# Performance work log

Measured on AMD Instinct MI355X. Metric: run time of the kernel, lower is better.

The kernel has to match this reference:

```python
import jax, jax.numpy as jnp
from jax import lax
import numpy as np

SOFT_LOCAL_MAX_SIZE = 3
PAD = SOFT_LOCAL_MAX_SIZE // 2


def setup_inputs() -> dict:
    key = jax.random.key(0)
    k1, k2 = jax.random.split(key)
    x = jax.random.normal(k1, (16, 64, 256, 256), dtype=jnp.float32)
    W = jax.random.normal(k2, (2, 64), dtype=jnp.float32) * 0.1  # 1x1 conv weight [out_c, in_c]
    b = jnp.zeros((2,), dtype=jnp.float32)
    return {"x": x, "W": W, "b": b}


def reference(x, W, b):
    # 1x1 conv == channel contraction
    y = jnp.einsum('bchw,oc->bohw', x, W) + b[None, :, None, None]
    e = jnp.exp(y)  # [B, 2, H, W]
    # replicate pad + 3x3 box SUM (avg_pool * k^2 == sum over window)
    p = jnp.pad(e, ((0, 0), (0, 0), (PAD, PAD), (PAD, PAD)), mode='edge')
    sum_exp = lax.reduce_window(
        p, jnp.float32(0.0), lax.add,
        window_dimensions=(1, 1, SOFT_LOCAL_MAX_SIZE, SOFT_LOCAL_MAX_SIZE),
        window_strides=(1, 1, 1, 1), padding='VALID')
    sum_exp = jnp.sum(sum_exp, axis=1, keepdims=True)  # channel sum -> [B,1,H,W]
    local_max_score = e / sum_exp
    return local_max_score[:, 0, :, :]  # [B, H, W]
```

## Files before the change

kernel.cpp:

```cpp
#include <hip/hip_runtime.h>
#include <math.h>

#define BB 16
#define CC 64
#define HH 256
#define WW 256
#define HWX (HH * WW)
#define NPIX (BB * HWX)

__global__ __launch_bounds__(256) void conv_exp_kernel(
    const float* __restrict__ x,
    const float* __restrict__ Wt,
    const float* __restrict__ bias,
    float* __restrict__ e0,
    float* __restrict__ s)
{
    __shared__ float w0[CC];
    __shared__ float w1[CC];
    const int tid = threadIdx.x;
    if (tid < CC) {
        w0[tid] = Wt[tid];
        w1[tid] = Wt[CC + tid];
    }
    __syncthreads();

    const float b0 = bias[0];
    const float b1 = bias[1];

    const long long p4 = (long long)blockIdx.x * blockDim.x + tid;
    const long long base = p4 * 4;
    if (base >= NPIX) return;
    const int bimg = (int)(base >> 16);
    const int q    = (int)(base & 65535);
    const float* xp = x + (long long)bimg * CC * HWX + q;

    float4 a0 = make_float4(b0, b0, b0, b0);
    float4 a1 = make_float4(b1, b1, b1, b1);

    #pragma unroll 8
    for (int c = 0; c < CC; ++c) {
        const float4 v = *(const float4*)(xp + (long long)c * HWX);
        const float wc0 = w0[c];
        const float wc1 = w1[c];
        a0.x = fmaf(v.x, wc0, a0.x);
        a0.y = fmaf(v.y, wc0, a0.y);
        a0.z = fmaf(v.z, wc0, a0.z);
        a0.w = fmaf(v.w, wc0, a0.w);
        a1.x = fmaf(v.x, wc1, a1.x);
        a1.y = fmaf(v.y, wc1, a1.y);
        a1.z = fmaf(v.z, wc1, a1.z);
        a1.w = fmaf(v.w, wc1, a1.w);
    }

    float4 E0, E1, S;
    E0.x = __expf(a0.x); E0.y = __expf(a0.y); E0.z = __expf(a0.z); E0.w = __expf(a0.w);
    E1.x = __expf(a1.x); E1.y = __expf(a1.y); E1.z = __expf(a1.z); E1.w = __expf(a1.w);
    S.x = E0.x + E1.x; S.y = E0.y + E1.y; S.z = E0.z + E1.z; S.w = E0.w + E1.w;

    *(float4*)(e0 + base) = E0;
    *(float4*)(s  + base) = S;
}

__global__ __launch_bounds__(256) void box_div_kernel(
    const float* __restrict__ e0,
    const float* __restrict__ s,
    float* __restrict__ out)
{
    const int idx = blockIdx.x * blockDim.x + threadIdx.x;
    if (idx >= NPIX) return;
    const int bimg = idx >> 16;
    const int q    = idx & 65535;
    const int h = q >> 8;
    const int w = q & 255;

    const int hm = (h > 0)      ? h - 1 : 0;
    const int hp = (h < HH - 1) ? h + 1 : HH - 1;
    const int wm = (w > 0)      ? w - 1 : 0;
    const int wp = (w < WW - 1) ? w + 1 : WW - 1;

    const float* sb = s + bimg * HWX;
    const int rm = hm * WW, r0 = h * WW, rp = hp * WW;

    const float sum =
        sb[rm + wm] + sb[rm + w] + sb[rm + wp] +
        sb[r0 + wm] + sb[r0 + w] + sb[r0 + wp] +
        sb[rp + wm] + sb[rp + w] + sb[rp + wp];

    out[idx] = e0[idx] / sum;
}

extern "C" void kernel_launch(void* const* d_in, const int* in_sizes, int n_in,
                              void* d_out, int out_size, void* d_ws, size_t ws_size,
                              hipStream_t stream) {
    const float* x    = (const float*)d_in[0];
    const float* Wt   = (const float*)d_in[1];
    const float* bias = (const float*)d_in[2];
    float* out = (float*)d_out;

    float* e0 = (float*)d_ws;
    float* s  = e0 + NPIX;

    {
        const int threads = 256;
        const int total = NPIX / 4;
        const int blocks = (total + threads - 1) / threads;
        conv_exp_kernel<<<blocks, threads, 0, stream>>>(x, Wt, bias, e0, s);
    }
    {
        const int threads = 256;
        const int blocks = (NPIX + threads - 1) / threads;
        box_div_kernel<<<blocks, threads, 0, stream>>>(e0, s, out);
    }
}
```

Measured before the change: 367.8 us.

## Fuse conv-exp and box-sum-divide into one row-tiled kernel with shared-memory halo

Replaces the two-kernel pipeline with a single kernel where each block computes a 16-row tile plus one halo row above and below. The block computes exp values into shared memory and then does the 3x3 box sum and divide locally. This removes the global write and re-read of the intermediate e0 and sum arrays and one kernel launch. In exchange it recomputes the channel contraction for halo rows (18/16 of the x reads) and launches only 256 large blocks of 576 threads, which may limit occupancy and latency hiding on the 64-channel read.

New measurement: 368.8 us. Within noise of the previous version (+0.3%).

```diff
diff --git a/kernel.cpp b/kernel.cpp
--- a/kernel.cpp
+++ b/kernel.cpp
@@ -1,92 +1,119 @@
 #include <hip/hip_runtime.h>
 #include <math.h>
 
-#define BB 16
 #define CC 64
 #define HH 256
 #define WW 256
 #define HWX (HH * WW)
-#define NPIX (BB * HWX)
+#define BB 16
+#define TH 16
+#define TROWS (TH + 2)
 
-__global__ __launch_bounds__(256) void conv_exp_kernel(
+__global__ __launch_bounds__(576) void fused_sdm_kernel(
     const float* __restrict__ x,
     const float* __restrict__ Wt,
     const float* __restrict__ bias,
-    float* __restrict__ e0,
-    float* __restrict__ s)
+    float* __restrict__ out)
 {
     __shared__ float w0[CC];
     __shared__ float w1[CC];
+    __shared__ float sS[TROWS][WW];
+    __shared__ float sE[TROWS][WW];
+
     const int tid = threadIdx.x;
-    if (tid < CC) {
-        w0[tid] = Wt[tid];
-        w1[tid] = Wt[CC + tid];
-    }
+    if (tid < CC)           w0[tid]      = Wt[tid];
+    else if (tid < 2 * CC)  w1[tid - CC] = Wt[tid];
     __syncthreads();
 
     const float b0 = bias[0];
     const float b1 = bias[1];
 
-    const long long p4 = (long long)blockIdx.x * blockDim.x + tid;
-    const long long base = p4 * 4;
-    if (base >= NPIX) return;
-    const int bimg = (int)(base >> 16);
-    const int q    = (int)(base & 65535);
-    const float* xp = x + (long long)bimg * CC * HWX + q;
+    const int bimg = blockIdx.x >> 4;
+    const int tile = blockIdx.x & 15;
+    const int h0   = tile * TH;
 
-    float4 a0 = make_float4(b0, b0, b0, b0);
-    float4 a1 = make_float4(b1, b1, b1, b1);
+    const int wg = tid & 63;
+    const int g  = tid >> 6;
+    const int w4 = wg << 2;
 
-    #pragma unroll 8
+    const int r0 = g;
+    const int r1 = g + 9;
+
+    int h_a = h0 + r0 - 1; h_a = h_a < 0 ? 0 : (h_a > HH - 1 ? HH - 1 : h_a);
+    int h_b = h0 + r1 - 1; h_b = h_b < 0 ? 0 : (h_b > HH - 1 ? HH - 1 : h_b);
+
+    const float* xb = x + (size_t)bimg * CC * HWX;
+    const int offA = h_a * WW + w4;
+    const int offB = h_b * WW + w4;
+
+    float4 A0 = make_float4(b0, b0, b0, b0);
+    float4 B0 = A0;
+    float4 A1 = make_float4(b1, b1, b1, b1);
+    float4 B1 = A1;
+
+    #pragma unroll 4
     for (int c = 0; c < CC; ++c) {
-        const float4 v = *(const float4*)(xp + (long long)c * HWX);
+        const float4 va = *(const float4*)(xb + (size_t)c * HWX + offA);
+        const float4 vb = *(const float4*)(xb + (size_t)c * HWX + offB);
         const float wc0 = w0[c];
         const float wc1 = w1[c];
-        a0.x = fmaf(v.x, wc0, a0.x);
-        a0.y = fmaf(v.y, wc0, a0.y);
-        a0.z = fmaf(v.z, wc0, a0.z);
-        a0.w = fmaf(v.w, wc0, a0.w);
-        a1.x = fmaf(v.x, wc1, a1.x);
-        a1.y = fmaf(v.y, wc1, a1.y);
-        a1.z = fmaf(v.z, wc1, a1.z);
-        a1.w = fmaf(v.w, wc1, a1.w);
+        A0.x = fmaf(va.x, wc0, A0.x);
+        A0.y = fmaf(va.y, wc0, A0.y);
+        A0.z = fmaf(va.z, wc0, A0.z);
+        A0.w = fmaf(va.w, wc0, A0.w);
+        A1.x = fmaf(va.x, wc1, A1.x);
+        A1.y = fmaf(va.y, wc1, A1.y);
+        A1.z = fmaf(va.z, wc1, A1.z);
+        A1.w = fmaf(va.w, wc1, A1.w);
+        B0.x = fmaf(vb.x, wc0, B0.x);
+        B0.y = fmaf(vb.y, wc0, B0.y);
+        B0.z = fmaf(vb.z, wc0, B0.z);
+        B0.w = fmaf(vb.w, wc0, B0.w);
+        B1.x = fmaf(vb.x, wc1, B1.x);
+        B1.y = fmaf(vb.y, wc1, B1.y);
+        B1.z = fmaf(vb.z, wc1, B1.z);
+        B1.w = fmaf(vb.w, wc1, B1.w);
     }
 
-    float4 E0, E1, S;
-    E0.x = __expf(a0.x); E0.y = __expf(a0.y); E0.z = __expf(a0.z); E0.w = __expf(a0.w);
-    E1.x = __expf(a1.x); E1.y = __expf(a1.y); E1.z = __expf(a1.z); E1.w = __expf(a1.w);
-    S.x = E0.x + E1.x; S.y = E0.y + E1.y; S.z = E0.z + E1.z; S.w = E0.w + E1.w;
+    float4 EA, EB, SA, SB;
+    EA.x = __expf(A0.x); EA.y = __expf(A0.y); EA.z = __expf(A0.z); EA.w = __expf(A0.w);
+    EB.x = __expf(B0.x); EB.y = __expf(B0.y); EB.z = __expf(B0.z); EB.w = __expf(B0.w);
+    SA.x = EA.x + __expf(A1.x); SA.y = EA.y + __expf(A1.y);
+    SA.z = EA.z + __expf(A1.z); SA.w = EA.w + __expf(A1.w);
+    SB.x = EB.x + __expf(B1.x); SB.y = EB.y + __expf(B1.y);
+    SB.z = EB.z + __expf(B1.z); SB.w = EB.w + __expf(B1.w);
 
-    *(float4*)(e0 + base) = E0;
-    *(float4*)(s  + base) = S;
-}
+    *(float4*)&sE[r0][w4] = EA;
+    *(float4*)&sS[r0][w4] = SA;
+    *(float4*)&sE[r1][w4] = EB;
+    *(float4*)&sS[r1][w4] = SB;
+    __syncthreads();
 
-__global__ __launch_bounds__(256) void box_div_kernel(
-    const float* __restrict__ e0,
-    const float* __restrict__ s,
-    float* __restrict__ out)
-{
-    const int idx = blockIdx.x * blockDim.x + threadIdx.x;
-    if (idx >= NPIX) return;
-    const int bimg = idx >> 16;
-    const int q    = idx & 65535;
-    const int h = q >> 8;
-    const int w = q & 255;
+    const int wl = (wg == 0)  ? 0      : w4 - 1;
+    const int wr = (wg == 63) ? WW - 1 : w4 + 4;
+    float* outb = out + (size_t)bimg * HWX;
 
-    const int hm = (h > 0)      ? h - 1 : 0;
-    const int hp = (h < HH - 1) ? h + 1 : HH - 1;
-    const int wm = (w > 0)      ? w - 1 : 0;
-    const int wp = (w < WW - 1) ? w + 1 : WW - 1;
+    #pragma unroll
+    for (int k = 0; k < 2; ++k) {
+        const int r = k ? r1 : r0;
+        if (r < 1 || r > TH) continue;
 
-    const float* sb = s + bimg * HWX;
-    const int rm = hm * WW, r0 = h * WW, rp = hp * WW;
-
-    const float sum =
-        sb[rm + wm] + sb[rm + w] + sb[rm + wp] +
-        sb[r0 + wm] + sb[r0 + w] + sb[r0 + wp] +
-        sb[rp + wm] + sb[rp + w] + sb[rp + wp];
-
-    out[idx] = e0[idx] / sum;
+        float cs0 = 0.f, cs1 = 0.f, cs2 = 0.f, cs3 = 0.f, cs4 = 0.f, cs5 = 0.f;
+        #pragma unroll
+        for (int dr = -1; dr <= 1; ++dr) {
+            const float4 m = *(const float4*)&sS[r + dr][w4];
+            cs0 += sS[r + dr][wl];
+            cs1 += m.x; cs2 += m.y; cs3 += m.z; cs4 += m.w;
+            cs5 += sS[r + dr][wr];
+        }
+        const float4 e = *(const float4*)&sE[r][w4];
+        float4 o;
+        o.x = e.x / (cs0 + cs1 + cs2);
+        o.y = e.y / (cs1 + cs2 + cs3);
+        o.z = e.z / (cs2 + cs3 + cs4);
+        o.w = e.w / (cs3 + cs4 + cs5);
+        *(float4*)(outb + (size_t)(h0 + r - 1) * WW + w4) = o;
+    }
 }
 
 extern "C" void kernel_launch(void* const* d_in, const int* in_sizes, int n_in,
@@ -97,18 +124,6 @@
     const float* bias = (const float*)d_in[2];
     float* out = (float*)d_out;
 
-    float* e0 = (float*)d_ws;
-    float* s  = e0 + NPIX;
-
-    {
-        const int threads = 256;
-        const int total = NPIX / 4;
-        const int blocks = (total + threads - 1) / threads;
-        conv_exp_kernel<<<blocks, threads, 0, stream>>>(x, Wt, bias, e0, s);
-    }
-    {
-        const int threads = 256;
-        const int blocks = (NPIX + threads - 1) / threads;
-        box_div_kernel<<<blocks, threads, 0, stream>>>(e0, s, out);
-    }
+    const int blocks = BB * (HH / TH);
+    fused_sdm_kernel<<<blocks, 576, 0, stream>>>(x, Wt, bias, out);
 }
```
